# Performance work log

Measured on AMD Instinct MI355X. Metric: run time of the kernel, lower is better.

## Reference

```python
import jax, jax.numpy as jnp
import numpy as np

MODEL_DIM = 512
NUM_HEADS = 8
HEAD_DIM = 64
INNER = NUM_HEADS * HEAD_DIM  # 512 == MODEL_DIM -> projection is Identity


def setup_inputs() -> dict:
    key = jax.random.key(0)
    ks = jax.random.split(key, 7)
    B, T = 2, 4096
    x = jax.random.normal(ks[0], (B, T, MODEL_DIM), dtype=jnp.float32)
    s = 1.0 / np.sqrt(MODEL_DIM)
    Wq = jax.random.normal(ks[1], (MODEL_DIM, INNER), dtype=jnp.float32) * s
    Wk = jax.random.normal(ks[2], (MODEL_DIM, INNER), dtype=jnp.float32) * s
    Wv = jax.random.normal(ks[3], (MODEL_DIM, INNER), dtype=jnp.float32) * s
    bq = jax.random.normal(ks[4], (INNER,), dtype=jnp.float32) * 0.01
    bk = jax.random.normal(ks[5], (INNER,), dtype=jnp.float32) * 0.01
    bv = jax.random.normal(ks[6], (INNER,), dtype=jnp.float32) * 0.01
    return {"x": x, "Wq": Wq, "bq": bq, "Wk": Wk, "bk": bk, "Wv": Wv, "bv": bv}


def reference(x, Wq, bq, Wk, bk, Wv, bv):
    B, T, _ = x.shape
    # project and split heads: [B, H, T, D]
    q = (x @ Wq + bq).reshape(B, T, NUM_HEADS, HEAD_DIM).transpose(0, 2, 1, 3)
    k = (x @ Wk + bk).reshape(B, T, NUM_HEADS, HEAD_DIM).transpose(0, 2, 1, 3)
    v = (x @ Wv + bv).reshape(B, T, NUM_HEADS, HEAD_DIM).transpose(0, 2, 1, 3)
    scale = 1.0 / np.sqrt(HEAD_DIM).astype(np.float32)
    attn = jnp.einsum('bhqd,bhkd->bhqk', q, k) * scale  # [B,H,Tq,Tkv]
    attn = jax.nn.softmax(attn, axis=-1)
    out = jnp.einsum('bhqk,bhkd->bhqd', attn, v)        # [B,H,Tq,D]
    out = out.transpose(0, 2, 1, 3).reshape(B, T, INNER)
    return out  # projection is Identity since INNER == MODEL_DIM
```

## Files before the change

### kernel.cpp

```cpp
#include <hip/hip_runtime.h>
#include <hip/hip_bf16.h>


typedef __attribute__((ext_vector_type(8)))  _Float16 half8;
typedef __attribute__((ext_vector_type(2)))  __fp16   fp16x2;
typedef __attribute__((ext_vector_type(4)))  float    f32x4;
typedef __attribute__((ext_vector_type(16))) float    f32x16;

#define TSEQ 4096
#define DH   64
#define NH   8
#define MD   512

#if __has_builtin(__builtin_amdgcn_exp2f)
__device__ inline float fexp2(float x){ return __builtin_amdgcn_exp2f(x); }
#else
__device__ inline float fexp2(float x){ float r; asm("v_exp_f32 %0, %1\n\ts_nop 1" : "=v"(r) : "v"(x)); return r; }
#endif

union H2U { fp16x2 h; unsigned int u; };
__device__ inline unsigned int pkrtz(float a, float b){
  H2U c; c.h = __builtin_amdgcn_cvt_pkrtz(a, b); return c.u;
}

union U4H8 { uint4 u; half8 h; };

#define AS3U(p) ((__attribute__((address_space(3))) unsigned int*)(p))
#define AS1U(p) ((const __attribute__((address_space(1))) unsigned int*)(p))

__global__ __launch_bounds__(256) void k_conv_x(const float* __restrict__ x, _Float16* __restrict__ xh){
  int i = (blockIdx.x*256 + threadIdx.x)*8;
  float4 a = *(const float4*)(x+i);
  float4 b = *(const float4*)(x+i+4);
  half8 o;
  o[0]=(_Float16)a.x; o[1]=(_Float16)a.y; o[2]=(_Float16)a.z; o[3]=(_Float16)a.w;
  o[4]=(_Float16)b.x; o[5]=(_Float16)b.y; o[6]=(_Float16)b.z; o[7]=(_Float16)b.w;
  *(half8*)(xh+i) = o;
}

__global__ __launch_bounds__(256) void k_prep_w(const float* __restrict__ Wq, const float* __restrict__ Wk,
                                                const float* __restrict__ Wv, _Float16* __restrict__ wt){
  __shared__ float tile[32][33];
  const int mat = blockIdx.z;
  const float* W = mat==0 ? Wq : (mat==1 ? Wk : Wv);
  const int n0 = blockIdx.x*32, k0 = blockIdx.y*32;
  const int tx = threadIdx.x & 31, ty = threadIdx.x >> 5;
  #pragma unroll
  for (int i=0;i<4;i++){ int k = ty*4+i; tile[k][tx] = W[(size_t)(k0+k)*MD + n0 + tx]; }
  __syncthreads();
  _Float16* dst = wt + (size_t)mat*MD*MD;
  #pragma unroll
  for (int i=0;i<4;i++){ int n = ty*4+i; dst[(size_t)(n0+n)*MD + k0 + tx] = (_Float16)tile[tx][n]; }
}

__global__ __launch_bounds__(256,2) void k_qkv(const _Float16* __restrict__ xh, const _Float16* __restrict__ wt,
              const float* __restrict__ bq, const float* __restrict__ bk, const float* __restrict__ bv,
              _Float16* __restrict__ qout, _Float16* __restrict__ kout, _Float16* __restrict__ vout){
  __shared__ _Float16 Ash[128*64];
  __shared__ _Float16 Bsh[128*64];
  const int tid = threadIdx.x, w = tid>>6, l = tid&63;
  const int fr = l&15, hi = l>>4;
  const int nt = blockIdx.x, mt = blockIdx.y;
  const int mat = nt>>2;
  const int n0  = (nt&3)*128;
  const int m0  = mt*128;
  const _Float16* W = wt + (size_t)mat*MD*MD;
  const int wr = (w>>1)*64, wc = (w&1)*64;

  f32x4 acc[4][4];
  #pragma unroll
  for (int a=0;a<4;a++)
    #pragma unroll
    for (int b=0;b<4;b++) acc[a][b] = (f32x4){0.f,0.f,0.f,0.f};

  for (int k0=0;k0<MD;k0+=64){
    #pragma unroll
    for (int i=0;i<4;i++){
      int slot = tid + i*256;
      int row = slot>>3, seg = slot&7;
      int sw = row*64 + ((seg ^ (row&7))<<3);
      *(half8*)&Ash[sw] = *(const half8*)(xh + (size_t)(m0+row)*MD + k0 + seg*8);
      *(half8*)&Bsh[sw] = *(const half8*)(W  + (size_t)(n0+row)*MD + k0 + seg*8);
    }
    __syncthreads();
    #pragma unroll
    for (int ks=0;ks<2;ks++){
      half8 af[4], bfr[4];
      #pragma unroll
      for (int mi=0;mi<4;mi++){
        int row = wr + mi*16 + fr;
        af[mi] = *(const half8*)&Ash[row*64 + (((ks*4+hi) ^ (row&7))<<3)];
      }
      #pragma unroll
      for (int ni=0;ni<4;ni++){
        int row = wc + ni*16 + fr;
        bfr[ni] = *(const half8*)&Bsh[row*64 + (((ks*4+hi) ^ (row&7))<<3)];
      }
      #pragma unroll
      for (int mi=0;mi<4;mi++)
        #pragma unroll
        for (int ni=0;ni<4;ni++)
          acc[mi][ni] = __builtin_amdgcn_mfma_f32_16x16x32_f16(af[mi], bfr[ni], acc[mi][ni], 0,0,0);
    }
    __syncthreads();
  }

  const float* bias = mat==0 ? bq : (mat==1 ? bk : bv);
  const float scl = (mat==0) ? 0.125f*1.4426950408889634f : (mat==2 ? 0.0625f : 1.0f);
  if (mat==1){
    #pragma unroll
    for (int ni=0;ni<4;ni++){
      int n_in = n0 + wc + ni*16 + fr;
      float bb = bias[n_in];
      int h = n_in>>6, d = n_in&63;
      #pragma unroll
      for (int mi=0;mi<4;mi++)
        #pragma unroll
        for (int r=0;r<4;r++){
          int m = m0 + wr + mi*16 + hi*4 + r;
          float v = acc[mi][ni][r] + bb;
          int b_ = m>>12, t = m&4095;
          kout[ ((((size_t)(b_*NH + h))*8 + (d>>3))*TSEQ + t)*8 + (d&7) ] = (_Float16)v;
        }
    }
  } else {
    _Float16* dst = mat==0 ? qout : vout;
    #pragma unroll
    for (int ni=0;ni<4;ni++){
      int n_in = n0 + wc + ni*16 + fr;
      float bb = bias[n_in];
      int h = n_in>>6, d = n_in&63;
      #pragma unroll
      for (int mi=0;mi<4;mi++)
        #pragma unroll
        for (int r=0;r<4;r++){
          int m = m0 + wr + mi*16 + hi*4 + r;
          float v = (acc[mi][ni][r] + bb)*scl;
          int b_ = m>>12, t = m&4095;
          dst[ ((size_t)((b_*NH + h)*TSEQ + t))*DH + d ] = (_Float16)v;
        }
    }
  }
}

__global__ __launch_bounds__(256) void k_trans_v(const _Float16* __restrict__ v, _Float16* __restrict__ vtg){
  __shared__ _Float16 tile[64][72];
  const int tid = threadIdx.x;
  const int bh = blockIdx.y, t0 = blockIdx.x*64;
  const _Float16* src = v + ((size_t)bh*TSEQ + t0)*DH;
  #pragma unroll
  for (int i=0;i<2;i++){
    int slot = tid + i*256; int r = slot>>3, s = slot&7;
    *(half8*)&tile[r][s*8] = *(const half8*)(src + (size_t)r*DH + s*8);
  }
  __syncthreads();
  #pragma unroll
  for (int i=0;i<2;i++){
    int slot = tid + i*256;
    int d = slot&63, sg = slot>>6;
    half8 o;
    #pragma unroll
    for (int j=0;j<8;j++) o[j] = tile[sg*8+j][d];
    *(half8*)(vtg + (((size_t)bh*512 + (t0>>3) + sg)*64 + d)*8) = o;
  }
}

__global__ __launch_bounds__(256,2) void k_attn(const _Float16* __restrict__ qb_, const _Float16* __restrict__ ktg,
                                                const _Float16* __restrict__ vtg, float* __restrict__ out){
  __shared__ alignas(16) _Float16 Ksh[2*8192];
  __shared__ alignas(16) _Float16 Vsh[2*8192];
  const int tid = threadIdx.x, w = tid>>6, l = tid&63;
  const int ln31 = l&31, lh = l>>5;

  const int bid = blockIdx.x;
  const int swz = ((bid&7)<<6) | (bid>>3);
  const int bh = swz>>5, qblk = swz&31;

  const _Float16* Q  = qb_ + (size_t)bh*TSEQ*DH;
  const _Float16* Kt = ktg + (size_t)bh*8*TSEQ*8;
  const _Float16* Vt = vtg + (size_t)bh*512*64*8;
  const int q0 = qblk*128 + w*32;

  half8 qf[4];
  #pragma unroll
  for (int ds=0;ds<4;ds++)
    qf[ds] = *(const half8*)(Q + (size_t)(q0 + ln31)*DH + ds*16 + lh*8);

  f32x16 of0, of1, sacc;
  #pragma unroll
  for (int r=0;r<16;r++){ of0[r]=0.f; of1[r]=0.f; sacc[r]=0.f; }
  const half8 onesv = {(_Float16)1,(_Float16)1,(_Float16)1,(_Float16)1,
                       (_Float16)1,(_Float16)1,(_Float16)1,(_Float16)1};

  const int NT = TSEQ/128;
  const int kbase = lh*1024 + ln31*8;
  const int vbase = lh*512  + ln31*8;

#define STAGE(kt, buf) do { \
    const int k0_ = (kt)*128; \
    _Pragma("unroll") \
    for (int i_=0;i_<4;i_++){ \
      int base_ = i_*256 + w*64; \
      int slot_ = base_ + l; \
      int krow_ = slot_&127, kseg_ = slot_>>7; \
      __builtin_amdgcn_global_load_lds(AS1U(Kt + ((size_t)kseg_*TSEQ + k0_ + krow_)*8), \
          AS3U((char*)Ksh + (buf)*16384 + base_*16), 16, 0, 0); \
      __builtin_amdgcn_global_load_lds(AS1U(Vt + ((size_t)slot_ + k0_*8)*8), \
          AS3U((char*)Vsh + (buf)*16384 + base_*16), 16, 0, 0); \
    } \
  } while(0)

  STAGE(0, 0);

  for (int kt=0; kt<NT; kt++){
    const int cur = kt&1;
    __syncthreads();
    if (kt+1 < NT) STAGE(kt+1, cur^1);

    const _Float16* Kb = &Ksh[cur*8192];
    const _Float16* Vb = &Vsh[cur*8192];

    #pragma unroll
    for (int kbq=0; kbq<4; kbq++){
      f32x16 s;
      #pragma unroll
      for (int r=0;r<16;r++) s[r]=0.f;
      #pragma unroll
      for (int ds=0;ds<4;ds++){
        half8 kf = *(const half8*)&Kb[kbase + ds*2048 + kbq*256];
        s = __builtin_amdgcn_mfma_f32_32x32x16_f16(kf, qf[ds], s, 0,0,0);
      }

      unsigned int wv[8];
      #pragma unroll
      for (int c=0;c<4;c++){
        float e0 = fexp2(s[4*c+0]);
        float e1 = fexp2(s[4*c+1]);
        float e2 = fexp2(s[4*c+2]);
        float e3 = fexp2(s[4*c+3]);
        wv[2*c+0] = pkrtz(e0, e1);
        wv[2*c+1] = pkrtz(e2, e3);
      }

      #pragma unroll
      for (int e=0;e<2;e++){
        unsigned int word[4];
        #pragma unroll
        for (int i=0;i<2;i++){
          unsigned int w0 = wv[4*e + i];
          unsigned int w1 = wv[4*e + 2 + i];
          unsigned int exp_ = (lh==0) ? w1 : w0;
          unsigned int cross = (unsigned int)__shfl((int)exp_, l ^ 32);
          word[i]   = (lh==0) ? w0 : cross;
          word[2+i] = (lh==0) ? cross : w1;
        }
        U4H8 pf; pf.u.x=word[0]; pf.u.y=word[1]; pf.u.z=word[2]; pf.u.w=word[3];
        sacc = __builtin_amdgcn_mfma_f32_32x32x16_f16(onesv, pf.h, sacc, 0,0,0);
        half8 v0 = *(const half8*)&Vb[vbase + kbq*2048 + e*1024];
        half8 v1 = *(const half8*)&Vb[vbase + kbq*2048 + e*1024 + 256];
        of0 = __builtin_amdgcn_mfma_f32_32x32x16_f16(v0, pf.h, of0, 0,0,0);
        of1 = __builtin_amdgcn_mfma_f32_32x32x16_f16(v1, pf.h, of1, 0,0,0);
      }
    }
  }

  float inv = 16.0f / sacc[0];

  const int b_ = bh>>3, h = bh&7;
  float* o = out + ((size_t)(b_*TSEQ + q0 + ln31))*MD + h*DH;
  #pragma unroll
  for (int rr=0;rr<4;rr++){
    float4 o4 = { of0[4*rr+0]*inv, of0[4*rr+1]*inv, of0[4*rr+2]*inv, of0[4*rr+3]*inv };
    *(float4*)(o + rr*8 + lh*4) = o4;
  }
  #pragma unroll
  for (int rr=0;rr<4;rr++){
    float4 o4 = { of1[4*rr+0]*inv, of1[4*rr+1]*inv, of1[4*rr+2]*inv, of1[4*rr+3]*inv };
    *(float4*)(o + 32 + rr*8 + lh*4) = o4;
  }
#undef STAGE
}

extern "C" void kernel_launch(void* const* d_in, const int* in_sizes, int n_in,
                              void* d_out, int out_size, void* d_ws, size_t ws_size,
                              hipStream_t stream) {
  const float* x  = (const float*)d_in[0];
  const float* Wq = (const float*)d_in[1];
  const float* bq = (const float*)d_in[2];
  const float* Wk = (const float*)d_in[3];
  const float* bk = (const float*)d_in[4];
  const float* Wv = (const float*)d_in[5];
  const float* bv = (const float*)d_in[6];
  float* out = (float*)d_out;

  char* ws = (char*)d_ws;
  _Float16* xh = (_Float16*)(ws);
  _Float16* wt = (_Float16*)(ws + ((size_t)8<<20));
  _Float16* qb = (_Float16*)(ws + ((size_t)10<<20));
  _Float16* kb = (_Float16*)(ws + ((size_t)18<<20));
  _Float16* vb = (_Float16*)(ws + ((size_t)26<<20));
  _Float16* vt = xh;

  k_conv_x<<<2048, 256, 0, stream>>>(x, xh);
  k_prep_w<<<dim3(16,16,3), 256, 0, stream>>>(Wq, Wk, Wv, wt);
  k_qkv<<<dim3(12,64), 256, 0, stream>>>(xh, wt, bq, bk, bv, qb, kb, vb);
  k_trans_v<<<dim3(64,16), 256, 0, stream>>>(vb, vt);
  k_attn<<<512, 256, 0, stream>>>(qb, kb, vt, out);
}
```

Baseline: 135.7 us.

## Double-buffer QKV GEMM via direct global-to-LDS loads and add MFMA setprio in attention

The QKV projection GEMM now uses two LDS buffers, filled with global_load_lds direct copies, so the next K-slice loads while MFMAs run on the current one. This removes one barrier per iteration and the register round-trip on staging. The attention loop also wraps its MFMA groups in s_setprio to raise wave priority during matrix work, which should help interleave exp/shuffle work across waves. The extra buffer doubles GEMM LDS use and may lower occupancy.

Measured after the change: 139.6 us. 1.03x slower.

```diff
diff --git a/kernel.cpp b/kernel.cpp
--- a/kernel.cpp
+++ b/kernel.cpp
@@ -56,8 +56,8 @@
 __global__ __launch_bounds__(256,2) void k_qkv(const _Float16* __restrict__ xh, const _Float16* __restrict__ wt,
               const float* __restrict__ bq, const float* __restrict__ bk, const float* __restrict__ bv,
               _Float16* __restrict__ qout, _Float16* __restrict__ kout, _Float16* __restrict__ vout){
-  __shared__ _Float16 Ash[128*64];
-  __shared__ _Float16 Bsh[128*64];
+  __shared__ alignas(16) _Float16 Ash[2][128*64];
+  __shared__ alignas(16) _Float16 Bsh[2][128*64];
   const int tid = threadIdx.x, w = tid>>6, l = tid&63;
   const int fr = l&15, hi = l>>4;
   const int nt = blockIdx.x, mt = blockIdx.y;
@@ -73,28 +73,38 @@
     #pragma unroll
     for (int b=0;b<4;b++) acc[a][b] = (f32x4){0.f,0.f,0.f,0.f};
 
-  for (int k0=0;k0<MD;k0+=64){
-    #pragma unroll
-    for (int i=0;i<4;i++){
-      int slot = tid + i*256;
-      int row = slot>>3, seg = slot&7;
-      int sw = row*64 + ((seg ^ (row&7))<<3);
-      *(half8*)&Ash[sw] = *(const half8*)(xh + (size_t)(m0+row)*MD + k0 + seg*8);
-      *(half8*)&Bsh[sw] = *(const half8*)(W  + (size_t)(n0+row)*MD + k0 + seg*8);
-    }
+#define QSTAGE(k0_, buf) do { \
+    _Pragma("unroll") \
+    for (int i_=0;i_<4;i_++){ \
+      int slot_ = tid + i_*256; \
+      int row_ = slot_>>3, seg_ = (slot_&7) ^ (row_&7); \
+      __builtin_amdgcn_global_load_lds(AS1U(xh + (size_t)(m0+row_)*MD + (k0_) + seg_*8), \
+          AS3U((char*)&Ash[buf][0] + slot_*16), 16, 0, 0); \
+      __builtin_amdgcn_global_load_lds(AS1U(W + (size_t)(n0+row_)*MD + (k0_) + seg_*8), \
+          AS3U((char*)&Bsh[buf][0] + slot_*16), 16, 0, 0); \
+    } \
+  } while(0)
+
+  QSTAGE(0, 0);
+
+  for (int ks0=0; ks0<8; ks0++){
+    const int cur = ks0&1;
     __syncthreads();
+    if (ks0+1 < 8) QSTAGE((ks0+1)*64, cur^1);
+    const _Float16* Ab = &Ash[cur][0];
+    const _Float16* Bb = &Bsh[cur][0];
     #pragma unroll
     for (int ks=0;ks<2;ks++){
       half8 af[4], bfr[4];
       #pragma unroll
       for (int mi=0;mi<4;mi++){
         int row = wr + mi*16 + fr;
-        af[mi] = *(const half8*)&Ash[row*64 + (((ks*4+hi) ^ (row&7))<<3)];
+        af[mi] = *(const half8*)&Ab[row*64 + (((ks*4+hi) ^ (row&7))<<3)];
       }
       #pragma unroll
       for (int ni=0;ni<4;ni++){
         int row = wc + ni*16 + fr;
-        bfr[ni] = *(const half8*)&Bsh[row*64 + (((ks*4+hi) ^ (row&7))<<3)];
+        bfr[ni] = *(const half8*)&Bb[row*64 + (((ks*4+hi) ^ (row&7))<<3)];
       }
       #pragma unroll
       for (int mi=0;mi<4;mi++)
@@ -102,8 +112,8 @@
         for (int ni=0;ni<4;ni++)
           acc[mi][ni] = __builtin_amdgcn_mfma_f32_16x16x32_f16(af[mi], bfr[ni], acc[mi][ni], 0,0,0);
     }
-    __syncthreads();
-  }
+  }
+#undef QSTAGE
 
   const float* bias = mat==0 ? bq : (mat==1 ? bk : bv);
   const float scl = (mat==0) ? 0.125f*1.4426950408889634f : (mat==2 ? 0.0625f : 1.0f);
@@ -225,11 +235,13 @@
       f32x16 s;
       #pragma unroll
       for (int r=0;r<16;r++) s[r]=0.f;
+      __builtin_amdgcn_s_setprio(1);
       #pragma unroll
       for (int ds=0;ds<4;ds++){
         half8 kf = *(const half8*)&Kb[kbase + ds*2048 + kbq*256];
         s = __builtin_amdgcn_mfma_f32_32x32x16_f16(kf, qf[ds], s, 0,0,0);
       }
+      __builtin_amdgcn_s_setprio(0);
 
       unsigned int wv[8];
       #pragma unroll
@@ -255,11 +267,13 @@
           word[2+i] = (lh==0) ? cross : w1;
         }
         U4H8 pf; pf.u.x=word[0]; pf.u.y=word[1]; pf.u.z=word[2]; pf.u.w=word[3];
-        sacc = __builtin_amdgcn_mfma_f32_32x32x16_f16(onesv, pf.h, sacc, 0,0,0);
         half8 v0 = *(const half8*)&Vb[vbase + kbq*2048 + e*1024];
         half8 v1 = *(const half8*)&Vb[vbase + kbq*2048 + e*1024 + 256];
+        __builtin_amdgcn_s_setprio(1);
+        sacc = __builtin_amdgcn_mfma_f32_32x32x16_f16(onesv, pf.h, sacc, 0,0,0);
         of0 = __builtin_amdgcn_mfma_f32_32x32x16_f16(v0, pf.h, of0, 0,0,0);
         of1 = __builtin_amdgcn_mfma_f32_32x32x16_f16(v1, pf.h, of1, 0,0,0);
+        __builtin_amdgcn_s_setprio(0);
       }
     }
   }
```
